# Performance work log

Hardware: AMD Instinct MI355X
Metric: run time of the kernel (lower is better)

Reference implementation:

```python
import jax, jax.numpy as jnp
import numpy as np

THRESHOLD = 3.0
MAX_POINTS = 200000


def setup_inputs() -> dict:
    key = jax.random.key(0)
    frames = jax.random.normal(key, (4, 8, 2, 4, 480, 640), dtype=jnp.float32)
    return {"frames": frames}


def reference(frames):
    # frames: [B, S, N_evt, C_evt, H, W]
    B, S, N_evt, C_evt, H, W = frames.shape
    C = N_evt * C_evt
    dense = frames.reshape(B * S, C, H, W)

    # threshold > 0 branch: channel-wise abs-max reduction then threshold
    mask = jnp.max(jnp.abs(dense), axis=1) > THRESHOLD  # [B*S, H, W]

    # jit-compatible compaction: fixed-capacity nonzero (row-major order,
    # deterministic truncation to MAX_POINTS replaces torch's randperm subsample)
    bf, y, x = jnp.nonzero(mask, size=MAX_POINTS, fill_value=0)
    n_valid = jnp.minimum(jnp.sum(mask), MAX_POINTS)
    valid = jnp.arange(MAX_POINTS) < n_valid  # [cap]

    batch_idx = bf // S
    time_idx = bf % S
    coords = jnp.stack((batch_idx, time_idx, y, x), axis=1).astype(jnp.int32)
    coords = jnp.where(valid[:, None], coords, 0)

    features = dense[bf, :, y, x]  # [cap, C] scattered gather
    features = jnp.where(valid[:, None], features, 0.0)

    return features, coords
```

## Files before the change

### kernel.cpp

```cpp
#include <hip/hip_runtime.h>
#include <hip/hip_bf16.h>

#define HW        307200
#define W_IMG     640
#define PIXELS    9830400
#define NBLK      38400
#define MAXPTS    200000
#define FEAT_OFF  0
#define COORD_OFF 1600000


__global__ __launch_bounds__(256) void mask_kernel(const float* __restrict__ frames,
                                                   unsigned long long* __restrict__ maskWords,
                                                   unsigned* __restrict__ blockCounts) {
    int tid   = threadIdx.x;
    int pixel = blockIdx.x * 256 + tid;
    int bf  = pixel / HW;
    int rem = pixel - bf * HW;
    const float* base = frames + (size_t)bf * 8 * HW + rem;
    float m = 0.0f;
#pragma unroll
    for (int c = 0; c < 8; ++c) m = fmaxf(m, fabsf(base[(size_t)c * HW]));
    bool pass = m > 3.0f;
    unsigned long long b = __ballot(pass);
    int wave = tid >> 6, lane = tid & 63;
    __shared__ unsigned cnt[4];
    if (lane == 0) {
        maskWords[(size_t)blockIdx.x * 4 + wave] = b;
        cnt[wave] = (unsigned)__popcll(b);
    }
    __syncthreads();
    if (tid == 0) blockCounts[blockIdx.x] = cnt[0] + cnt[1] + cnt[2] + cnt[3];
}

__global__ __launch_bounds__(256) void scan_kernel(const unsigned* __restrict__ counts,
                                                   unsigned* __restrict__ offsets) {
    __shared__ unsigned s[256];
    int tid = threadIdx.x;
    const int per = (NBLK + 255) / 256;
    int begin = tid * per;
    int end   = begin + per > NBLK ? NBLK : begin + per;
    unsigned sum = 0;
    for (int i = begin; i < end; ++i) sum += counts[i];
    s[tid] = sum;
    __syncthreads();
    if (tid == 0) {
        unsigned acc = 0;
        for (int i = 0; i < 256; ++i) { unsigned v = s[i]; s[i] = acc; acc += v; }
    }
    __syncthreads();
    unsigned acc = s[tid];
    for (int i = begin; i < end; ++i) { offsets[i] = acc; acc += counts[i]; }
}

__global__ __launch_bounds__(256) void emit_kernel(const float* __restrict__ frames,
                                                   const unsigned long long* __restrict__ maskWords,
                                                   const unsigned* __restrict__ blockOffsets,
                                                   float* __restrict__ out) {
    int tid  = threadIdx.x;
    int wave = tid >> 6, lane = tid & 63;

    __shared__ unsigned wcnt[4];
    __shared__ unsigned long long words[4];
    if (tid < 4) {
        unsigned long long w = maskWords[(size_t)blockIdx.x * 4 + tid];
        words[tid] = w;
        wcnt[tid]  = (unsigned)__popcll(w);
    }
    __syncthreads();

    unsigned long long word = words[wave];
    bool pass = (word >> lane) & 1ULL;
    if (!pass) return;

    unsigned before = 0;
    for (int w = 0; w < wave; ++w) before += wcnt[w];
    unsigned rankInWave = (unsigned)__popcll(word & ((1ULL << lane) - 1ULL));
    unsigned rank = blockOffsets[blockIdx.x] + before + rankInWave;
    if (rank >= MAXPTS) return;

    int pixel = blockIdx.x * 256 + tid;
    int bf  = pixel / HW;
    int rem = pixel - bf * HW;
    int y   = rem / W_IMG;
    int x   = rem - y * W_IMG;

    const float* base = frames + (size_t)bf * 8 * HW + rem;
    float* fo = out + FEAT_OFF + (size_t)rank * 8;
#pragma unroll
    for (int c = 0; c < 8; ++c) fo[c] = base[(size_t)c * HW];

    float* co = out + COORD_OFF + (size_t)rank * 4;
    co[0] = (float)(bf >> 3);
    co[1] = (float)(bf & 7);
    co[2] = (float)y;
    co[3] = (float)x;
}

extern "C" void kernel_launch(void* const* d_in, const int* in_sizes, int n_in,
                              void* d_out, int out_size, void* d_ws, size_t ws_size,
                              hipStream_t stream) {
    const float* frames = (const float*)d_in[0];
    float* out = (float*)d_out;

    char* ws = (char*)d_ws;
    unsigned long long* maskWords = (unsigned long long*)(ws);
    unsigned* blockCounts  = (unsigned*)(ws + 1228800);
    unsigned* blockOffsets = (unsigned*)(ws + 1382400);

    hipMemsetAsync(d_out, 0, (size_t)out_size * sizeof(float), stream);

    mask_kernel<<<NBLK, 256, 0, stream>>>(frames, maskWords, blockCounts);
    scan_kernel<<<1, 256, 0, stream>>>(blockCounts, blockOffsets);
    emit_kernel<<<NBLK, 256, 0, stream>>>(frames, maskWords, blockOffsets, out);
}
```

Measured before the change: 502.9 us.

## Fuse mask, scan and emit into single-pass decoupled look-back kernel

Replaces the three-kernel mask/scan/emit pipeline with one kernel. Each tile loads 8 channels as float4 vectors, computes the threshold mask, and gets its global offset through a decoupled look-back prefix scan, using atomic tile tickets and per-tile status words. Features and coords are written straight from registers. This removes the second read of the frames and the serial single-block scan, at the cost of spin-wait look-back chains and an extra workspace memset.

```diff
diff --git a/kernel.cpp b/kernel.cpp
--- a/kernel.cpp
+++ b/kernel.cpp
@@ -1,100 +1,139 @@
 #include <hip/hip_runtime.h>
 #include <hip/hip_bf16.h>
+#include <stdint.h>
 
 #define HW        307200
 #define W_IMG     640
-#define PIXELS    9830400
-#define NBLK      38400
+#define TILE      1024
+#define NTILES    9600
+#define BLK_PER_BF 300
 #define MAXPTS    200000
-#define FEAT_OFF  0
 #define COORD_OFF 1600000
 
 
-__global__ __launch_bounds__(256) void mask_kernel(const float* __restrict__ frames,
-                                                   unsigned long long* __restrict__ maskWords,
-                                                   unsigned* __restrict__ blockCounts) {
-    int tid   = threadIdx.x;
-    int pixel = blockIdx.x * 256 + tid;
-    int bf  = pixel / HW;
-    int rem = pixel - bf * HW;
-    const float* base = frames + (size_t)bf * 8 * HW + rem;
-    float m = 0.0f;
+__device__ __forceinline__ unsigned waveSum(unsigned v) {
 #pragma unroll
-    for (int c = 0; c < 8; ++c) m = fmaxf(m, fabsf(base[(size_t)c * HW]));
-    bool pass = m > 3.0f;
-    unsigned long long b = __ballot(pass);
-    int wave = tid >> 6, lane = tid & 63;
-    __shared__ unsigned cnt[4];
-    if (lane == 0) {
-        maskWords[(size_t)blockIdx.x * 4 + wave] = b;
-        cnt[wave] = (unsigned)__popcll(b);
+    for (int off = 32; off >= 1; off >>= 1)
+        v += __shfl_xor(v, off, 64);
+    return v;
+}
+
+__device__ __forceinline__ float comp4(const float4& q, int i) {
+    return i == 0 ? q.x : i == 1 ? q.y : i == 2 ? q.z : q.w;
+}
+
+__global__ __launch_bounds__(256) void fused_voxelizer(
+        const float* __restrict__ frames, float* __restrict__ out,
+        unsigned* __restrict__ ticket, unsigned long long* __restrict__ status) {
+    __shared__ unsigned s_tile;
+    __shared__ unsigned s_wsum[4];
+    __shared__ unsigned s_prefix;
+
+    int tid  = threadIdx.x;
+    int lane = tid & 63, wave = tid >> 6;
+
+    if (tid == 0) s_tile = atomicAdd(ticket, 1u);
+    __syncthreads();
+    unsigned tile = s_tile;
+
+    int bf      = (int)(tile / BLK_PER_BF);
+    int pixBase = (int)(tile - (unsigned)bf * BLK_PER_BF) * TILE + tid * 4;
+    const float* base = frames + (size_t)bf * (8 * (size_t)HW) + pixBase;
+
+    float4 v[8];
+#pragma unroll
+    for (int c = 0; c < 8; ++c)
+        v[c] = *(const float4*)(base + (size_t)c * HW);
+
+    float m0 = 0.f, m1 = 0.f, m2 = 0.f, m3 = 0.f;
+#pragma unroll
+    for (int c = 0; c < 8; ++c) {
+        m0 = fmaxf(m0, fabsf(v[c].x));
+        m1 = fmaxf(m1, fabsf(v[c].y));
+        m2 = fmaxf(m2, fabsf(v[c].z));
+        m3 = fmaxf(m3, fabsf(v[c].w));
+    }
+    int k0 = m0 > 3.0f, k1 = m1 > 3.0f, k2 = m2 > 3.0f, k3 = m3 > 3.0f;
+    unsigned cnt = (unsigned)(k0 + k1 + k2 + k3);
+
+    unsigned inc = cnt;
+#pragma unroll
+    for (int off = 1; off < 64; off <<= 1) {
+        unsigned n = __shfl_up(inc, off, 64);
+        if (lane >= off) inc += n;
+    }
+    if (lane == 63) s_wsum[wave] = inc;
+    __syncthreads();
+    unsigned wbase = 0;
+#pragma unroll
+    for (int w = 0; w < 4; ++w)
+        if (w < wave) wbase += s_wsum[w];
+    unsigned total = s_wsum[0] + s_wsum[1] + s_wsum[2] + s_wsum[3];
+    unsigned excl  = wbase + inc - cnt;
+
+    if (wave == 0) {
+        if (lane == 0)
+            __hip_atomic_store(&status[tile],
+                               (1ull << 32) | (unsigned long long)total,
+                               __ATOMIC_RELEASE, __HIP_MEMORY_SCOPE_AGENT);
+        unsigned pfx = 0;
+        int end = (int)tile;
+        while (end > 0) {
+            int idx = end - 64 + lane;
+            bool have = idx >= 0;
+            unsigned long long s = 0;
+            while (true) {
+                if (have && (s >> 32) == 0)
+                    s = __hip_atomic_load(&status[idx], __ATOMIC_ACQUIRE,
+                                          __HIP_MEMORY_SCOPE_AGENT);
+                bool ok = !have || (s >> 32) != 0;
+                if (__ballot(ok) == ~0ull) break;
+                __builtin_amdgcn_s_sleep(1);
+            }
+            unsigned long long pmask = __ballot(have && (s >> 32) == 2);
+            if (pmask) {
+                int lp = 63 - __clzll(pmask);
+                unsigned contrib = (have && lane >= lp) ? (unsigned)s : 0;
+                pfx += waveSum(contrib);
+                break;
+            } else {
+                unsigned contrib = have ? (unsigned)s : 0;
+                pfx += waveSum(contrib);
+                end -= 64;
+            }
+        }
+        if (lane == 0) {
+            __hip_atomic_store(&status[tile],
+                               (2ull << 32) | (unsigned long long)(pfx + total),
+                               __ATOMIC_RELEASE, __HIP_MEMORY_SCOPE_AGENT);
+            s_prefix = pfx;
+        }
     }
     __syncthreads();
-    if (tid == 0) blockCounts[blockIdx.x] = cnt[0] + cnt[1] + cnt[2] + cnt[3];
-}
+    unsigned r = s_prefix + excl;
 
-__global__ __launch_bounds__(256) void scan_kernel(const unsigned* __restrict__ counts,
-                                                   unsigned* __restrict__ offsets) {
-    __shared__ unsigned s[256];
-    int tid = threadIdx.x;
-    const int per = (NBLK + 255) / 256;
-    int begin = tid * per;
-    int end   = begin + per > NBLK ? NBLK : begin + per;
-    unsigned sum = 0;
-    for (int i = begin; i < end; ++i) sum += counts[i];
-    s[tid] = sum;
-    __syncthreads();
-    if (tid == 0) {
-        unsigned acc = 0;
-        for (int i = 0; i < 256; ++i) { unsigned v = s[i]; s[i] = acc; acc += v; }
+    int k[4] = {k0, k1, k2, k3};
+#pragma unroll
+    for (int i = 0; i < 4; ++i) {
+        if (k[i]) {
+            if (r < MAXPTS) {
+                float f0 = comp4(v[0], i), f1 = comp4(v[1], i);
+                float f2 = comp4(v[2], i), f3 = comp4(v[3], i);
+                float f4 = comp4(v[4], i), f5 = comp4(v[5], i);
+                float f6 = comp4(v[6], i), f7 = comp4(v[7], i);
+                float4* fo = (float4*)(out + (size_t)r * 8);
+                fo[0] = make_float4(f0, f1, f2, f3);
+                fo[1] = make_float4(f4, f5, f6, f7);
+                int pix = pixBase + i;
+                int y = pix / W_IMG;
+                int x = pix - y * W_IMG;
+                float4* co = (float4*)(out + COORD_OFF) + r;
+                *co = make_float4((float)(bf >> 3), (float)(bf & 7),
+                                  (float)y, (float)x);
+            }
+            r++;
+        }
     }
-    __syncthreads();
-    unsigned acc = s[tid];
-    for (int i = begin; i < end; ++i) { offsets[i] = acc; acc += counts[i]; }
-}
-
-__global__ __launch_bounds__(256) void emit_kernel(const float* __restrict__ frames,
-                                                   const unsigned long long* __restrict__ maskWords,
-                                                   const unsigned* __restrict__ blockOffsets,
-                                                   float* __restrict__ out) {
-    int tid  = threadIdx.x;
-    int wave = tid >> 6, lane = tid & 63;
-
-    __shared__ unsigned wcnt[4];
-    __shared__ unsigned long long words[4];
-    if (tid < 4) {
-        unsigned long long w = maskWords[(size_t)blockIdx.x * 4 + tid];
-        words[tid] = w;
-        wcnt[tid]  = (unsigned)__popcll(w);
-    }
-    __syncthreads();
-
-    unsigned long long word = words[wave];
-    bool pass = (word >> lane) & 1ULL;
-    if (!pass) return;
-
-    unsigned before = 0;
-    for (int w = 0; w < wave; ++w) before += wcnt[w];
-    unsigned rankInWave = (unsigned)__popcll(word & ((1ULL << lane) - 1ULL));
-    unsigned rank = blockOffsets[blockIdx.x] + before + rankInWave;
-    if (rank >= MAXPTS) return;
-
-    int pixel = blockIdx.x * 256 + tid;
-    int bf  = pixel / HW;
-    int rem = pixel - bf * HW;
-    int y   = rem / W_IMG;
-    int x   = rem - y * W_IMG;
-
-    const float* base = frames + (size_t)bf * 8 * HW + rem;
-    float* fo = out + FEAT_OFF + (size_t)rank * 8;
-#pragma unroll
-    for (int c = 0; c < 8; ++c) fo[c] = base[(size_t)c * HW];
-
-    float* co = out + COORD_OFF + (size_t)rank * 4;
-    co[0] = (float)(bf >> 3);
-    co[1] = (float)(bf & 7);
-    co[2] = (float)y;
-    co[3] = (float)x;
 }
 
 extern "C" void kernel_launch(void* const* d_in, const int* in_sizes, int n_in,
@@ -104,13 +143,11 @@
     float* out = (float*)d_out;
 
     char* ws = (char*)d_ws;
-    unsigned long long* maskWords = (unsigned long long*)(ws);
-    unsigned* blockCounts  = (unsigned*)(ws + 1228800);
-    unsigned* blockOffsets = (unsigned*)(ws + 1382400);
+    unsigned* ticket = (unsigned*)ws;
+    unsigned long long* status = (unsigned long long*)(ws + 64);
 
+    hipMemsetAsync(d_ws, 0, 64 + (size_t)NTILES * 8, stream);
     hipMemsetAsync(d_out, 0, (size_t)out_size * sizeof(float), stream);
 
-    mask_kernel<<<NBLK, 256, 0, stream>>>(frames, maskWords, blockCounts);
-    scan_kernel<<<1, 256, 0, stream>>>(blockCounts, blockOffsets);
-    emit_kernel<<<NBLK, 256, 0, stream>>>(frames, maskWords, blockOffsets, out);
+    fused_voxelizer<<<NTILES, 256, 0, stream>>>(frames, out, ticket, status);
 }
```

Result: slower. 1.470 ms (+192.3%).
